# Performance work log

Measured on AMD Instinct MI355X. Metric: run time of the kernel, lower is better.

The kernel has to match this reference:

```python
import jax, jax.numpy as jnp
import numpy as np

B, S, H, T, NF = 64, 512, 1024, 4, 12
P = NF * (NF - 1) // 2  # 66 step pairs


def _head(x, w1, b1, w2, b2):
    # LinearsHead (eval mode: dropout = identity): linear -> relu -> linear
    return jax.nn.relu(x @ w1 + b1) @ w2 + b2


def setup_inputs() -> dict:
    key = jax.random.key(0)
    ks = jax.random.split(key, 12)
    sc = 0.02
    # non-overlapping contiguous spans: targets then facts, each L tokens
    L = S // (T + NF)  # 32
    t_start = jnp.arange(T, dtype=jnp.int32) * L
    f_start = (T + jnp.arange(NF, dtype=jnp.int32)) * L
    target_offsets = jnp.broadcast_to(jnp.stack([t_start, t_start + L], -1), (B, T, 2))
    fact_offsets = jnp.broadcast_to(jnp.stack([f_start, f_start + L], -1), (B, NF, 2))
    return {
        'seq_features': jax.random.normal(ks[0], (B, S, H), jnp.float32),
        'cls_features': jax.random.normal(ks[1], (B, H), jnp.float32),
        'target_offsets': target_offsets,
        'fact_offsets': fact_offsets,
        'fact_score_mask': jnp.ones((B, NF, T), jnp.float32),
        'sentsim_w1': sc * jax.random.normal(ks[2], (2 * H, H), jnp.float32),
        'sentsim_b1': jnp.zeros((H,), jnp.float32),
        'sentsim_w2': sc * jax.random.normal(ks[3], (H, 1), jnp.float32),
        'sentsim_b2': jnp.zeros((1,), jnp.float32),
        'step_w1': sc * jax.random.normal(ks[4], (2 * H, H), jnp.float32),
        'step_b1': jnp.zeros((H,), jnp.float32),
        'step_w2': sc * jax.random.normal(ks[5], (H, 1), jnp.float32),
        'step_b2': jnp.zeros((1,), jnp.float32),
        'state_w1': sc * jax.random.normal(ks[6], (H, H), jnp.float32),
        'state_b1': jnp.zeros((H,), jnp.float32),
        'state_w2': sc * jax.random.normal(ks[7], (H, 1), jnp.float32),
        'state_b2': jnp.zeros((1,), jnp.float32),
        'abd_w1': sc * jax.random.normal(ks[8], (2 * H, H), jnp.float32),
        'abd_b1': jnp.zeros((H,), jnp.float32),
        'abd_w2': sc * jax.random.normal(ks[9], (H, 1), jnp.float32),
        'abd_b2': jnp.zeros((1,), jnp.float32),
        'lambda_weight': jnp.array([0.5, 0.5], jnp.float32),
    }


def reference(seq_features, cls_features, target_offsets, fact_offsets, fact_score_mask,
              sentsim_w1, sentsim_b1, sentsim_w2, sentsim_b2,
              step_w1, step_b1, step_w2, step_b2,
              state_w1, state_b1, state_w2, state_b2,
              abd_w1, abd_b1, abd_w2, abd_b2, lambda_weight):
    b, s, h = seq_features.shape
    t = target_offsets.shape[1]
    nf = fact_offsets.shape[1]
    pos = jnp.arange(s)

    def seg_mean(offs):  # offs [b,k,2] -> mean-pooled [b,k,h]
        m = ((pos >= offs[..., 0:1]) & (pos < offs[..., 1:2])).astype(seq_features.dtype)
        cnt = (offs[..., 1] - offs[..., 0]).astype(seq_features.dtype)[..., None]
        return jnp.einsum('bks,bsh->bkh', m, seq_features) / cnt

    tgt = seg_mean(target_offsets)  # [b,t,h]
    fct = seg_mean(fact_offsets)    # [b,nf,h]

    # fact-cls pairs ordered target-major: features[ti*nf+fi] = cat(fact, target)
    ff = jnp.broadcast_to(fct[:, None], (b, t, nf, h))
    tt = jnp.broadcast_to(tgt[:, :, None], (b, t, nf, h))
    pair = jnp.concatenate([ff, tt], -1).reshape(b, t * nf, 2 * h)
    fact_score = jax.nn.sigmoid(_head(pair, sentsim_w1, sentsim_b1, sentsim_w2, sentsim_b2)[..., 0])  # [b, t*nf]
    # original does .view(len(facts), len(targets)) on the flat t-major scores
    mat = fact_score.reshape(b, nf, t)
    max_per_fact = jnp.max(mat * fact_score_mask, axis=2)  # [b, nf]
    state_fact = jnp.mean(max_per_fact, axis=1)            # [b]
    state_cls = jax.nn.sigmoid(_head(cls_features, state_w1, state_b1, state_w2, state_b2)[..., 0])
    w = jax.nn.softmax(lambda_weight)
    state = w[0] * state_fact + w[1] * state_cls           # [b]

    # step pairs: combinations(range(nf), 2) == row-major triu indices
    i1, i2 = jnp.triu_indices(nf, k=1)
    step_feat = jnp.concatenate([fct[:, i1], fct[:, i2]], -1)  # [b,P,2h]
    step = _head(step_feat, step_w1, step_b1, step_w2, step_b2)[..., 0]  # [b,P]

    tside = jnp.mean(tgt, axis=1)  # sum/len over targets [b,h]
    abd_feat = jnp.concatenate([jnp.broadcast_to(tside[:, None], (b, nf, h)), fct], -1)
    abd = _head(abd_feat, abd_w1, abd_b1, abd_w2, abd_b2)[..., 0]  # [b,nf]

    # step_func == 'softmax_all': joint softmax over step + abd scores
    allsc = jax.nn.softmax(jnp.concatenate([step, abd], axis=1), axis=1)
    np_pairs = i1.shape[0]
    step, abd = allsc[:, :np_pairs], allsc[:, np_pairs:]

    # pack: [state | fact_score | step | step_abd]
    return jnp.concatenate([state[:, None], fact_score, step, abd], axis=1)
```

## Files before the change

kernel.cpp:

```cpp
#include <hip/hip_runtime.h>
#include <hip/hip_bf16.h>

#define B_    64
#define S_    512
#define H_    1024
#define HH_   (H_*H_)
#define T_    4
#define NF_   12
#define TNF_  48
#define NP_   66
#define OUTC_ 127

#define NSENT_ (B_*TNF_)
#define NSTEP_ (B_*NP_)
#define NABD_  (B_*NF_)
#define NCLS_  (B_)
#define NWAVES_ (NSENT_+NSTEP_+NABD_+NCLS_)

#define AROW_FCT   0
#define AROW_TGT   768
#define AROW_TSD   1024
#define AROW_CLS   1088
#define AROWS_     1152

#define GROW_FSENT 0
#define GROW_S1    768
#define GROW_S2    1536
#define GROW_AF    2304
#define GROW_TSENT 3072
#define GROW_AT    3328
#define GROW_CLS   3392
#define GROWS_     3456

typedef __bf16 bf16x8 __attribute__((ext_vector_type(8)));
typedef float  f32x4  __attribute__((ext_vector_type(4)));
typedef __attribute__((address_space(1))) const unsigned int gcu32;
typedef __attribute__((address_space(3))) unsigned int lu32;

__device__ __forceinline__ ushort f2bf(float x) {
    union { float f; unsigned u; } c; c.f = x;
    unsigned r = c.u + 0x7fffu + ((c.u >> 16) & 1u);
    return (ushort)(r >> 16);
}
__device__ __forceinline__ float bflo(unsigned u) {
    union { unsigned u; float f; } c; c.u = u << 16; return c.f;
}
__device__ __forceinline__ float bfhi(unsigned u) {
    union { unsigned u; float f; } c; c.u = u & 0xffff0000u; return c.f;
}

__global__ __launch_bounds__(256) void seg_mean_kernel(
    const float* __restrict__ seq, const int* __restrict__ toffs,
    const int* __restrict__ foffs, float* __restrict__ tgt32,
    ushort* __restrict__ Abf)
{
    int blk = blockIdx.x;
    int b = blk >> 4;
    int k = blk & 15;
    int start, end, arow;
    float* dst32 = nullptr;
    if (k < T_) {
        start = toffs[(b*T_ + k)*2];
        end   = toffs[(b*T_ + k)*2 + 1];
        dst32 = tgt32 + (size_t)(b*T_ + k) * H_;
        arow  = AROW_TGT + b*T_ + k;
    } else {
        int f = k - T_;
        start = foffs[(b*NF_ + f)*2];
        end   = foffs[(b*NF_ + f)*2 + 1];
        arow  = AROW_FCT + b*NF_ + f;
    }
    int h0 = threadIdx.x * 4;
    const float* base = seq + ((size_t)b * S_ + start) * H_ + h0;
    float4 s = make_float4(0.f, 0.f, 0.f, 0.f);
    int n = end - start;
    for (int r = 0; r < n; ++r) {
        float4 v = *(const float4*)(base + (size_t)r * H_);
        s.x += v.x; s.y += v.y; s.z += v.z; s.w += v.w;
    }
    float inv = 1.f / (float)n;
    s.x *= inv; s.y *= inv; s.z *= inv; s.w *= inv;
    if (dst32) *(float4*)(dst32 + h0) = s;
    ushort4 q; q.x = f2bf(s.x); q.y = f2bf(s.y); q.z = f2bf(s.z); q.w = f2bf(s.w);
    *(ushort4*)(Abf + (size_t)arow * H_ + h0) = q;
}

__global__ __launch_bounds__(256) void tside_cls_kernel(
    const float* __restrict__ tgt32, const float* __restrict__ cls,
    ushort* __restrict__ Abf)
{
    int b = blockIdx.x;
    int h0 = threadIdx.x * 4;
    float4 s = make_float4(0.f, 0.f, 0.f, 0.f);
    for (int t = 0; t < T_; ++t) {
        float4 v = *(const float4*)(tgt32 + (size_t)(b*T_ + t)*H_ + h0);
        s.x += v.x; s.y += v.y; s.z += v.z; s.w += v.w;
    }
    ushort4 q;
    q.x = f2bf(s.x*0.25f); q.y = f2bf(s.y*0.25f);
    q.z = f2bf(s.z*0.25f); q.w = f2bf(s.w*0.25f);
    *(ushort4*)(Abf + (size_t)(AROW_TSD + b) * H_ + h0) = q;
    float4 c = *(const float4*)(cls + (size_t)b * H_ + h0);
    ushort4 qc; qc.x = f2bf(c.x); qc.y = f2bf(c.y); qc.z = f2bf(c.z); qc.w = f2bf(c.w);
    *(ushort4*)(Abf + (size_t)(AROW_CLS + b) * H_ + h0) = qc;
}

__global__ __launch_bounds__(256) void transpose_cast_kernel(
    const float* __restrict__ sw1, const float* __restrict__ pw1,
    const float* __restrict__ aw1, const float* __restrict__ cw1,
    ushort* __restrict__ Wt)
{
    __shared__ float Tt[32][33];
    int z = blockIdx.z;
    const float* src;
    switch (z) {
        case 0: src = sw1; break;
        case 1: src = pw1; break;
        case 2: src = pw1 + HH_; break;
        case 3: src = aw1 + HH_; break;
        case 4: src = sw1 + HH_; break;
        case 5: src = aw1; break;
        default: src = cw1; break;
    }
    int k0 = blockIdx.x * 32;
    int n0 = blockIdx.y * 32;
    int tid = threadIdx.x;
    int ty = tid >> 3, tx = tid & 7;
    float4 v = *(const float4*)(src + (size_t)(k0 + ty) * H_ + n0 + tx*4);
    Tt[ty][tx*4 + 0] = v.x; Tt[ty][tx*4 + 1] = v.y;
    Tt[ty][tx*4 + 2] = v.z; Tt[ty][tx*4 + 3] = v.w;
    __syncthreads();
    int nx = ty, kx = tx;
    ushort4 q;
    q.x = f2bf(Tt[kx*4 + 0][nx]); q.y = f2bf(Tt[kx*4 + 1][nx]);
    q.z = f2bf(Tt[kx*4 + 2][nx]); q.w = f2bf(Tt[kx*4 + 3][nx]);
    *(ushort4*)(Wt + (size_t)z * HH_ + (size_t)(n0 + nx) * H_ + k0 + kx*4) = q;
}

__global__ __launch_bounds__(256) void gemm_bf16_kernel(
    const ushort* __restrict__ Abf, const ushort* __restrict__ Wt,
    ushort* __restrict__ G)
{
    __shared__ __align__(16) ushort As[64*32];
    __shared__ __align__(16) ushort Bs[64*32];

    int bx = blockIdx.x;
    int arow_base, wsel, grow_base, mt;
    if (bx < 48)      { int j = bx / 12; mt = bx % 12; arow_base = AROW_FCT; wsel = j; grow_base = j * 768; }
    else if (bx < 52) { mt = bx - 48; arow_base = AROW_TGT; wsel = 4; grow_base = GROW_TSENT; }
    else if (bx == 52){ mt = 0; arow_base = AROW_TSD; wsel = 5; grow_base = GROW_AT; }
    else              { mt = 0; arow_base = AROW_CLS; wsel = 6; grow_base = GROW_CLS; }

    const int tid  = threadIdx.x;
    const int lane = tid & 63;
    const int w    = tid >> 6;
    const int wr   = w >> 1, wc = w & 1;
    const int m0   = mt * 64;
    const int n0   = blockIdx.y * 64;

    const int srow   = lane >> 2;
    const int scol8  = (lane & 3) * 8;
    const ushort* gA = Abf + (size_t)(arow_base + m0 + w*16 + srow) * H_ + scol8;
    const ushort* gB = Wt + (size_t)wsel * HH_ + (size_t)(n0 + w*16 + srow) * H_ + scol8;
    ushort* ldsA = As + w * 512;
    ushort* ldsB = Bs + w * 512;

    f32x4 acc00 = {0.f,0.f,0.f,0.f}, acc01 = {0.f,0.f,0.f,0.f};
    f32x4 acc10 = {0.f,0.f,0.f,0.f}, acc11 = {0.f,0.f,0.f,0.f};

    const int frow = lane & 15;
    const int fk   = (lane >> 4) * 8;
    const ushort* pa = As + (wr*32 + frow) * 32 + fk;
    const ushort* pb = Bs + (wc*32 + frow) * 32 + fk;

    for (int k0 = 0; k0 < H_; k0 += 32) {
        __syncthreads();
        __builtin_amdgcn_global_load_lds((gcu32*)(gA + k0), (lu32*)ldsA, 16, 0, 0);
        __builtin_amdgcn_global_load_lds((gcu32*)(gB + k0), (lu32*)ldsB, 16, 0, 0);
        __syncthreads();

        bf16x8 a0 = *(const bf16x8*)pa;
        bf16x8 a1 = *(const bf16x8*)(pa + 16*32);
        bf16x8 b0 = *(const bf16x8*)pb;
        bf16x8 b1 = *(const bf16x8*)(pb + 16*32);

        acc00 = __builtin_amdgcn_mfma_f32_16x16x32_bf16(a0, b0, acc00, 0, 0, 0);
        acc01 = __builtin_amdgcn_mfma_f32_16x16x32_bf16(a0, b1, acc01, 0, 0, 0);
        acc10 = __builtin_amdgcn_mfma_f32_16x16x32_bf16(a1, b0, acc10, 0, 0, 0);
        acc11 = __builtin_amdgcn_mfma_f32_16x16x32_bf16(a1, b1, acc11, 0, 0, 0);
    }

    const int r0 = (lane >> 4) * 4;
    const int c  = lane & 15;
    const size_t rowb = (size_t)(grow_base + m0 + wr*32);
    #pragma unroll
    for (int r = 0; r < 4; ++r) {
        G[(rowb + 0  + r0 + r) * H_ + n0 + wc*32 + 0  + c] = f2bf(acc00[r]);
        G[(rowb + 0  + r0 + r) * H_ + n0 + wc*32 + 16 + c] = f2bf(acc01[r]);
        G[(rowb + 16 + r0 + r) * H_ + n0 + wc*32 + 0  + c] = f2bf(acc10[r]);
        G[(rowb + 16 + r0 + r) * H_ + n0 + wc*32 + 16 + c] = f2bf(acc11[r]);
    }
}

__global__ __launch_bounds__(256) void combine_kernel(
    const ushort* __restrict__ G,
    const float* __restrict__ sb1, const float* __restrict__ sw2,
    const float* __restrict__ pb1, const float* __restrict__ pw2,
    const float* __restrict__ ab1, const float* __restrict__ aw2,
    const float* __restrict__ cb1, const float* __restrict__ cw2,
    float* __restrict__ ssent, float* __restrict__ sstep,
    float* __restrict__ sabd, float* __restrict__ scls)
{
    int wv = blockIdx.x * 4 + (threadIdx.x >> 6);
    int lane = threadIdx.x & 63;
    if (wv >= NWAVES_) return;

    const ushort *U, *V;
    const float *b1, *w2;
    float* outp;
    if (wv < NSENT_) {
        int b = wv / TNF_, q = wv % TNF_;
        int t = q / NF_, f = q % NF_;
        U = G + (size_t)(GROW_FSENT + b*NF_ + f) * H_;
        V = G + (size_t)(GROW_TSENT + b*T_ + t) * H_;
        b1 = sb1; w2 = sw2; outp = ssent + wv;
    } else if (wv < NSENT_ + NSTEP_) {
        int s = wv - NSENT_;
        int b = s / NP_, p = s % NP_;
        int i = 0, rem = p, cnt = NF_ - 1;
        while (rem >= cnt) { rem -= cnt; --cnt; ++i; }
        int j = i + 1 + rem;
        U = G + (size_t)(GROW_S1 + b*NF_ + i) * H_;
        V = G + (size_t)(GROW_S2 + b*NF_ + j) * H_;
        b1 = pb1; w2 = pw2; outp = sstep + s;
    } else if (wv < NSENT_ + NSTEP_ + NABD_) {
        int s = wv - NSENT_ - NSTEP_;
        int b = s / NF_, f = s % NF_;
        U = G + (size_t)(GROW_AT + b) * H_;
        V = G + (size_t)(GROW_AF + b*NF_ + f) * H_;
        b1 = ab1; w2 = aw2; outp = sabd + s;
    } else {
        int b = wv - NSENT_ - NSTEP_ - NABD_;
        U = G + (size_t)(GROW_CLS + b) * H_;
        V = nullptr;
        b1 = cb1; w2 = cw2; outp = scls + b;
    }

    float acc = 0.f;
    #pragma unroll
    for (int h = 0; h < 2; ++h) {
        int nb = h * 512 + lane * 8;
        uint4 uu = *(const uint4*)(U + nb);
        float us[8] = { bflo(uu.x), bfhi(uu.x), bflo(uu.y), bfhi(uu.y),
                        bflo(uu.z), bfhi(uu.z), bflo(uu.w), bfhi(uu.w) };
        if (V) {
            uint4 vv = *(const uint4*)(V + nb);
            us[0] += bflo(vv.x); us[1] += bfhi(vv.x);
            us[2] += bflo(vv.y); us[3] += bfhi(vv.y);
            us[4] += bflo(vv.z); us[5] += bfhi(vv.z);
            us[6] += bflo(vv.w); us[7] += bfhi(vv.w);
        }
        float4 bA = *(const float4*)(b1 + nb);
        float4 bB = *(const float4*)(b1 + nb + 4);
        float4 wA = *(const float4*)(w2 + nb);
        float4 wB = *(const float4*)(w2 + nb + 4);
        acc = fmaf(fmaxf(us[0] + bA.x, 0.f), wA.x, acc);
        acc = fmaf(fmaxf(us[1] + bA.y, 0.f), wA.y, acc);
        acc = fmaf(fmaxf(us[2] + bA.z, 0.f), wA.z, acc);
        acc = fmaf(fmaxf(us[3] + bA.w, 0.f), wA.w, acc);
        acc = fmaf(fmaxf(us[4] + bB.x, 0.f), wB.x, acc);
        acc = fmaf(fmaxf(us[5] + bB.y, 0.f), wB.y, acc);
        acc = fmaf(fmaxf(us[6] + bB.z, 0.f), wB.z, acc);
        acc = fmaf(fmaxf(us[7] + bB.w, 0.f), wB.w, acc);
    }
    #pragma unroll
    for (int msk = 1; msk < 64; msk <<= 1)
        acc += __shfl_xor(acc, msk);
    if (lane == 0) *outp = acc;
}

__global__ __launch_bounds__(128) void finalize_kernel(
    const float* __restrict__ s_sent, const float* __restrict__ s_step,
    const float* __restrict__ s_abd, const float* __restrict__ s_cls,
    const float* __restrict__ mask, const float* __restrict__ lam,
    const float* __restrict__ sent_b2, const float* __restrict__ step_b2,
    const float* __restrict__ state_b2, const float* __restrict__ abd_b2,
    float* __restrict__ out)
{
    int b = blockIdx.x;
    int tid = threadIdx.x;
    __shared__ float fs[TNF_];
    __shared__ float sc[NP_ + NF_];
    __shared__ float mpf[NF_];
    __shared__ float smax, ssum;

    if (tid < TNF_) {
        float v = 1.f / (1.f + expf(-(s_sent[b*TNF_ + tid] + sent_b2[0])));
        fs[tid] = v;
        out[(size_t)b*OUTC_ + 1 + tid] = v;
    }
    if (tid < NP_)
        sc[tid] = s_step[b*NP_ + tid] + step_b2[0];
    else if (tid < NP_ + NF_)
        sc[tid] = s_abd[b*NF_ + (tid - NP_)] + abd_b2[0];
    __syncthreads();

    if (tid < NF_) {
        float m = -1e30f;
        for (int j = 0; j < T_; ++j)
            m = fmaxf(m, fs[tid*T_ + j] * mask[((size_t)b*NF_ + tid)*T_ + j]);
        mpf[tid] = m;
    }
    __syncthreads();

    if (tid == 0) {
        float sf = 0.f;
        for (int i = 0; i < NF_; ++i) sf += mpf[i];
        sf *= (1.f / NF_);
        float scls2 = 1.f / (1.f + expf(-(s_cls[b] + state_b2[0])));
        float l0 = lam[0], l1 = lam[1];
        float mx = fmaxf(l0, l1);
        float e0 = expf(l0 - mx), e1 = expf(l1 - mx);
        float w0 = e0 / (e0 + e1);
        out[(size_t)b*OUTC_] = w0 * sf + (1.f - w0) * scls2;
        float m2 = -1e30f;
        for (int i = 0; i < NP_ + NF_; ++i) m2 = fmaxf(m2, sc[i]);
        smax = m2;
    }
    __syncthreads();
    if (tid < NP_ + NF_) sc[tid] = expf(sc[tid] - smax);
    __syncthreads();
    if (tid == 0) {
        float s2 = 0.f;
        for (int i = 0; i < NP_ + NF_; ++i) s2 += sc[i];
        ssum = s2;
    }
    __syncthreads();
    if (tid < NP_ + NF_)
        out[(size_t)b*OUTC_ + 1 + TNF_ + tid] = sc[tid] / ssum;
}

extern "C" void kernel_launch(void* const* d_in, const int* in_sizes, int n_in,
                              void* d_out, int out_size, void* d_ws, size_t ws_size,
                              hipStream_t stream)
{
    (void)in_sizes; (void)n_in; (void)out_size; (void)ws_size;
    const float* seq  = (const float*)d_in[0];
    const float* cls  = (const float*)d_in[1];
    const int*   toff = (const int*)d_in[2];
    const int*   foff = (const int*)d_in[3];
    const float* mask = (const float*)d_in[4];
    const float* sw1  = (const float*)d_in[5];
    const float* sb1  = (const float*)d_in[6];
    const float* sw2  = (const float*)d_in[7];
    const float* sb2  = (const float*)d_in[8];
    const float* pw1  = (const float*)d_in[9];
    const float* pb1  = (const float*)d_in[10];
    const float* pw2  = (const float*)d_in[11];
    const float* pb2  = (const float*)d_in[12];
    const float* cw1  = (const float*)d_in[13];
    const float* cb1  = (const float*)d_in[14];
    const float* cw2  = (const float*)d_in[15];
    const float* cb2  = (const float*)d_in[16];
    const float* aw1  = (const float*)d_in[17];
    const float* ab1  = (const float*)d_in[18];
    const float* aw2  = (const float*)d_in[19];
    const float* ab2  = (const float*)d_in[20];
    const float* lam  = (const float*)d_in[21];

    char* wsb = (char*)d_ws;
    float*  tgt32 = (float*)wsb;
    float*  ssent = (float*)(wsb + (1u<<20));
    float*  sstep = ssent + NSENT_;
    float*  sabd  = sstep + NSTEP_;
    float*  scls  = sabd + NABD_;
    ushort* Abf   = (ushort*)(wsb + (1u<<20) + 32768);
    ushort* Wt    = Abf + (size_t)AROWS_ * H_;
    ushort* G     = Wt + (size_t)7 * HH_;

    seg_mean_kernel<<<B_*(T_ + NF_), 256, 0, stream>>>(seq, toff, foff, tgt32, Abf);
    tside_cls_kernel<<<B_, 256, 0, stream>>>(tgt32, cls, Abf);
    transpose_cast_kernel<<<dim3(32, 32, 7), 256, 0, stream>>>(sw1, pw1, aw1, cw1, Wt);

    gemm_bf16_kernel<<<dim3(54, 16), 256, 0, stream>>>(Abf, Wt, G);

    combine_kernel<<<(NWAVES_ + 3) / 4, 256, 0, stream>>>(
        G, sb1, sw2, pb1, pw2, ab1, aw2, cb1, cw2,
        ssent, sstep, sabd, scls);

    finalize_kernel<<<B_, 128, 0, stream>>>(
        ssent, sstep, sabd, scls, mask, lam, sb2, pb2, cb2, ab2, (float*)d_out);
}
```

Measured before the change: 65.65 us.

## Fuse prep kernels and double-buffer GEMM with wider 128-column tiles

Merges the segment-mean, cls cast and weight transpose-cast kernels into one launch so these independent memory-bound passes can run concurrently. Tside stays a separate small kernel. The bf16 GEMM now double-buffers its LDS staging, issuing the next k-tile's global-to-LDS loads before running MFMAs on the current one. It also widens the N tile to 128, giving 8 MFMAs per wave per step and halving the grid. The wider tile means fewer blocks (432) on a large-CU GPU, which may reduce occupancy.

```diff
diff --git a/kernel.cpp b/kernel.cpp
--- a/kernel.cpp
+++ b/kernel.cpp
@@ -49,45 +49,85 @@
     union { unsigned u; float f; } c; c.u = u & 0xffff0000u; return c.f;
 }
 
-__global__ __launch_bounds__(256) void seg_mean_kernel(
+__global__ __launch_bounds__(256) void prep_kernel(
     const float* __restrict__ seq, const int* __restrict__ toffs,
-    const int* __restrict__ foffs, float* __restrict__ tgt32,
-    ushort* __restrict__ Abf)
+    const int* __restrict__ foffs, const float* __restrict__ cls,
+    const float* __restrict__ sw1, const float* __restrict__ pw1,
+    const float* __restrict__ aw1, const float* __restrict__ cw1,
+    float* __restrict__ tgt32, ushort* __restrict__ Abf,
+    ushort* __restrict__ Wt)
 {
     int blk = blockIdx.x;
-    int b = blk >> 4;
-    int k = blk & 15;
-    int start, end, arow;
-    float* dst32 = nullptr;
-    if (k < T_) {
-        start = toffs[(b*T_ + k)*2];
-        end   = toffs[(b*T_ + k)*2 + 1];
-        dst32 = tgt32 + (size_t)(b*T_ + k) * H_;
-        arow  = AROW_TGT + b*T_ + k;
+    int tid = threadIdx.x;
+
+    if (blk < 1024) {
+        int b = blk >> 4;
+        int k = blk & 15;
+        int start, end, arow;
+        float* dst32 = nullptr;
+        if (k < T_) {
+            start = toffs[(b*T_ + k)*2];
+            end   = toffs[(b*T_ + k)*2 + 1];
+            dst32 = tgt32 + (size_t)(b*T_ + k) * H_;
+            arow  = AROW_TGT + b*T_ + k;
+        } else {
+            int f = k - T_;
+            start = foffs[(b*NF_ + f)*2];
+            end   = foffs[(b*NF_ + f)*2 + 1];
+            arow  = AROW_FCT + b*NF_ + f;
+        }
+        int h0 = tid * 4;
+        const float* base = seq + ((size_t)b * S_ + start) * H_ + h0;
+        float4 s = make_float4(0.f, 0.f, 0.f, 0.f);
+        int n = end - start;
+        #pragma unroll 4
+        for (int r = 0; r < n; ++r) {
+            float4 v = *(const float4*)(base + (size_t)r * H_);
+            s.x += v.x; s.y += v.y; s.z += v.z; s.w += v.w;
+        }
+        float inv = 1.f / (float)n;
+        s.x *= inv; s.y *= inv; s.z *= inv; s.w *= inv;
+        if (dst32) *(float4*)(dst32 + h0) = s;
+        ushort4 q; q.x = f2bf(s.x); q.y = f2bf(s.y); q.z = f2bf(s.z); q.w = f2bf(s.w);
+        *(ushort4*)(Abf + (size_t)arow * H_ + h0) = q;
+    } else if (blk < 1088) {
+        int b = blk - 1024;
+        int h0 = tid * 4;
+        float4 c = *(const float4*)(cls + (size_t)b * H_ + h0);
+        ushort4 qc; qc.x = f2bf(c.x); qc.y = f2bf(c.y); qc.z = f2bf(c.z); qc.w = f2bf(c.w);
+        *(ushort4*)(Abf + (size_t)(AROW_CLS + b) * H_ + h0) = qc;
     } else {
-        int f = k - T_;
-        start = foffs[(b*NF_ + f)*2];
-        end   = foffs[(b*NF_ + f)*2 + 1];
-        arow  = AROW_FCT + b*NF_ + f;
-    }
-    int h0 = threadIdx.x * 4;
-    const float* base = seq + ((size_t)b * S_ + start) * H_ + h0;
-    float4 s = make_float4(0.f, 0.f, 0.f, 0.f);
-    int n = end - start;
-    for (int r = 0; r < n; ++r) {
-        float4 v = *(const float4*)(base + (size_t)r * H_);
-        s.x += v.x; s.y += v.y; s.z += v.z; s.w += v.w;
-    }
-    float inv = 1.f / (float)n;
-    s.x *= inv; s.y *= inv; s.z *= inv; s.w *= inv;
-    if (dst32) *(float4*)(dst32 + h0) = s;
-    ushort4 q; q.x = f2bf(s.x); q.y = f2bf(s.y); q.z = f2bf(s.z); q.w = f2bf(s.w);
-    *(ushort4*)(Abf + (size_t)arow * H_ + h0) = q;
-}
-
-__global__ __launch_bounds__(256) void tside_cls_kernel(
-    const float* __restrict__ tgt32, const float* __restrict__ cls,
-    ushort* __restrict__ Abf)
+        __shared__ float Tt[32][33];
+        int idx2 = blk - 1088;
+        int z = idx2 >> 10;
+        int rem = idx2 & 1023;
+        int k0 = (rem >> 5) * 32;
+        int n0 = (rem & 31) * 32;
+        const float* src;
+        switch (z) {
+            case 0: src = sw1; break;
+            case 1: src = pw1; break;
+            case 2: src = pw1 + HH_; break;
+            case 3: src = aw1 + HH_; break;
+            case 4: src = sw1 + HH_; break;
+            case 5: src = aw1; break;
+            default: src = cw1; break;
+        }
+        int ty = tid >> 3, tx = tid & 7;
+        float4 v = *(const float4*)(src + (size_t)(k0 + ty) * H_ + n0 + tx*4);
+        Tt[ty][tx*4 + 0] = v.x; Tt[ty][tx*4 + 1] = v.y;
+        Tt[ty][tx*4 + 2] = v.z; Tt[ty][tx*4 + 3] = v.w;
+        __syncthreads();
+        int nx = ty, kx = tx;
+        ushort4 q;
+        q.x = f2bf(Tt[kx*4 + 0][nx]); q.y = f2bf(Tt[kx*4 + 1][nx]);
+        q.z = f2bf(Tt[kx*4 + 2][nx]); q.w = f2bf(Tt[kx*4 + 3][nx]);
+        *(ushort4*)(Wt + (size_t)z * HH_ + (size_t)(n0 + nx) * H_ + k0 + kx*4) = q;
+    }
+}
+
+__global__ __launch_bounds__(256) void tside_kernel(
+    const float* __restrict__ tgt32, ushort* __restrict__ Abf)
 {
     int b = blockIdx.x;
     int h0 = threadIdx.x * 4;
@@ -100,49 +140,14 @@
     q.x = f2bf(s.x*0.25f); q.y = f2bf(s.y*0.25f);
     q.z = f2bf(s.z*0.25f); q.w = f2bf(s.w*0.25f);
     *(ushort4*)(Abf + (size_t)(AROW_TSD + b) * H_ + h0) = q;
-    float4 c = *(const float4*)(cls + (size_t)b * H_ + h0);
-    ushort4 qc; qc.x = f2bf(c.x); qc.y = f2bf(c.y); qc.z = f2bf(c.z); qc.w = f2bf(c.w);
-    *(ushort4*)(Abf + (size_t)(AROW_CLS + b) * H_ + h0) = qc;
-}
-
-__global__ __launch_bounds__(256) void transpose_cast_kernel(
-    const float* __restrict__ sw1, const float* __restrict__ pw1,
-    const float* __restrict__ aw1, const float* __restrict__ cw1,
-    ushort* __restrict__ Wt)
-{
-    __shared__ float Tt[32][33];
-    int z = blockIdx.z;
-    const float* src;
-    switch (z) {
-        case 0: src = sw1; break;
-        case 1: src = pw1; break;
-        case 2: src = pw1 + HH_; break;
-        case 3: src = aw1 + HH_; break;
-        case 4: src = sw1 + HH_; break;
-        case 5: src = aw1; break;
-        default: src = cw1; break;
-    }
-    int k0 = blockIdx.x * 32;
-    int n0 = blockIdx.y * 32;
-    int tid = threadIdx.x;
-    int ty = tid >> 3, tx = tid & 7;
-    float4 v = *(const float4*)(src + (size_t)(k0 + ty) * H_ + n0 + tx*4);
-    Tt[ty][tx*4 + 0] = v.x; Tt[ty][tx*4 + 1] = v.y;
-    Tt[ty][tx*4 + 2] = v.z; Tt[ty][tx*4 + 3] = v.w;
-    __syncthreads();
-    int nx = ty, kx = tx;
-    ushort4 q;
-    q.x = f2bf(Tt[kx*4 + 0][nx]); q.y = f2bf(Tt[kx*4 + 1][nx]);
-    q.z = f2bf(Tt[kx*4 + 2][nx]); q.w = f2bf(Tt[kx*4 + 3][nx]);
-    *(ushort4*)(Wt + (size_t)z * HH_ + (size_t)(n0 + nx) * H_ + k0 + kx*4) = q;
 }
 
 __global__ __launch_bounds__(256) void gemm_bf16_kernel(
     const ushort* __restrict__ Abf, const ushort* __restrict__ Wt,
     ushort* __restrict__ G)
 {
-    __shared__ __align__(16) ushort As[64*32];
-    __shared__ __align__(16) ushort Bs[64*32];
+    __shared__ __align__(16) ushort As[2][64*32];
+    __shared__ __align__(16) ushort Bs[2][128*32];
 
     int bx = blockIdx.x;
     int arow_base, wsel, grow_base, mt;
@@ -156,49 +161,72 @@
     const int w    = tid >> 6;
     const int wr   = w >> 1, wc = w & 1;
     const int m0   = mt * 64;
-    const int n0   = blockIdx.y * 64;
-
-    const int srow   = lane >> 2;
-    const int scol8  = (lane & 3) * 8;
-    const ushort* gA = Abf + (size_t)(arow_base + m0 + w*16 + srow) * H_ + scol8;
-    const ushort* gB = Wt + (size_t)wsel * HH_ + (size_t)(n0 + w*16 + srow) * H_ + scol8;
-    ushort* ldsA = As + w * 512;
-    ushort* ldsB = Bs + w * 512;
-
-    f32x4 acc00 = {0.f,0.f,0.f,0.f}, acc01 = {0.f,0.f,0.f,0.f};
-    f32x4 acc10 = {0.f,0.f,0.f,0.f}, acc11 = {0.f,0.f,0.f,0.f};
+    const int n0   = blockIdx.y * 128;
+
+    const int srow  = lane >> 2;
+    const int scol8 = (lane & 3) * 8;
+    const ushort* gA  = Abf + (size_t)(arow_base + m0 + w*16 + srow) * H_ + scol8;
+    const ushort* gB0 = Wt + (size_t)wsel * HH_ + (size_t)(n0 + w*32 + srow) * H_ + scol8;
+    const ushort* gB1 = gB0 + (size_t)16 * H_;
+
+    f32x4 acc00 = {0,0,0,0}, acc01 = {0,0,0,0}, acc02 = {0,0,0,0}, acc03 = {0,0,0,0};
+    f32x4 acc10 = {0,0,0,0}, acc11 = {0,0,0,0}, acc12 = {0,0,0,0}, acc13 = {0,0,0,0};
 
     const int frow = lane & 15;
     const int fk   = (lane >> 4) * 8;
-    const ushort* pa = As + (wr*32 + frow) * 32 + fk;
-    const ushort* pb = Bs + (wc*32 + frow) * 32 + fk;
-
-    for (int k0 = 0; k0 < H_; k0 += 32) {
-        __syncthreads();
-        __builtin_amdgcn_global_load_lds((gcu32*)(gA + k0), (lu32*)ldsA, 16, 0, 0);
-        __builtin_amdgcn_global_load_lds((gcu32*)(gB + k0), (lu32*)ldsB, 16, 0, 0);
-        __syncthreads();
-
+
+    #define STAGE(buf, kk) do {                                                   \
+        __builtin_amdgcn_global_load_lds((gcu32*)(gA  + (kk)), (lu32*)(As[buf] + w*512), 16, 0, 0);          \
+        __builtin_amdgcn_global_load_lds((gcu32*)(gB0 + (kk)), (lu32*)(Bs[buf] + w*1024), 16, 0, 0);         \
+        __builtin_amdgcn_global_load_lds((gcu32*)(gB1 + (kk)), (lu32*)(Bs[buf] + w*1024 + 512), 16, 0, 0);   \
+    } while (0)
+
+    STAGE(0, 0);
+    __syncthreads();
+
+    #pragma unroll 1
+    for (int t = 0; t < 32; ++t) {
+        const int cur = t & 1;
+        if (t < 31) STAGE(cur ^ 1, (t + 1) * 32);
+
+        const ushort* pa = As[cur] + (wr*32 + frow) * 32 + fk;
+        const ushort* pb = Bs[cur] + (wc*64 + frow) * 32 + fk;
         bf16x8 a0 = *(const bf16x8*)pa;
-        bf16x8 a1 = *(const bf16x8*)(pa + 16*32);
+        bf16x8 a1 = *(const bf16x8*)(pa + 512);
         bf16x8 b0 = *(const bf16x8*)pb;
-        bf16x8 b1 = *(const bf16x8*)(pb + 16*32);
+        bf16x8 b1 = *(const bf16x8*)(pb + 512);
+        bf16x8 b2 = *(const bf16x8*)(pb + 1024);
+        bf16x8 b3 = *(const bf16x8*)(pb + 1536);
 
         acc00 = __builtin_amdgcn_mfma_f32_16x16x32_bf16(a0, b0, acc00, 0, 0, 0);
         acc01 = __builtin_amdgcn_mfma_f32_16x16x32_bf16(a0, b1, acc01, 0, 0, 0);
+        acc02 = __builtin_amdgcn_mfma_f32_16x16x32_bf16(a0, b2, acc02, 0, 0, 0);
+        acc03 = __builtin_amdgcn_mfma_f32_16x16x32_bf16(a0, b3, acc03, 0, 0, 0);
         acc10 = __builtin_amdgcn_mfma_f32_16x16x32_bf16(a1, b0, acc10, 0, 0, 0);
         acc11 = __builtin_amdgcn_mfma_f32_16x16x32_bf16(a1, b1, acc11, 0, 0, 0);
-    }
+        acc12 = __builtin_amdgcn_mfma_f32_16x16x32_bf16(a1, b2, acc12, 0, 0, 0);
+        acc13 = __builtin_amdgcn_mfma_f32_16x16x32_bf16(a1, b3, acc13, 0, 0, 0);
+
+        if (t < 31) __syncthreads();
+    }
+    #undef STAGE
 
     const int r0 = (lane >> 4) * 4;
     const int c  = lane & 15;
     const size_t rowb = (size_t)(grow_base + m0 + wr*32);
+    const size_t colb = (size_t)(n0 + wc*64);
     #pragma unroll
     for (int r = 0; r < 4; ++r) {
-        G[(rowb + 0  + r0 + r) * H_ + n0 + wc*32 + 0  + c] = f2bf(acc00[r]);
-        G[(rowb + 0  + r0 + r) * H_ + n0 + wc*32 + 16 + c] = f2bf(acc01[r]);
-        G[(rowb + 16 + r0 + r) * H_ + n0 + wc*32 + 0  + c] = f2bf(acc10[r]);
-        G[(rowb + 16 + r0 + r) * H_ + n0 + wc*32 + 16 + c] = f2bf(acc11[r]);
+        size_t ra = (rowb + r0 + r) * H_ + colb;
+        size_t rb = (rowb + 16 + r0 + r) * H_ + colb;
+        G[ra + 0  + c] = f2bf(acc00[r]);
+        G[ra + 16 + c] = f2bf(acc01[r]);
+        G[ra + 32 + c] = f2bf(acc02[r]);
+        G[ra + 48 + c] = f2bf(acc03[r]);
+        G[rb + 0  + c] = f2bf(acc10[r]);
+        G[rb + 16 + c] = f2bf(acc11[r]);
+        G[rb + 32 + c] = f2bf(acc12[r]);
+        G[rb + 48 + c] = f2bf(acc13[r]);
     }
 }
 
@@ -378,11 +406,12 @@
     ushort* Wt    = Abf + (size_t)AROWS_ * H_;
     ushort* G     = Wt + (size_t)7 * HH_;
 
-    seg_mean_kernel<<<B_*(T_ + NF_), 256, 0, stream>>>(seq, toff, foff, tgt32, Abf);
-    tside_cls_kernel<<<B_, 256, 0, stream>>>(tgt32, cls, Abf);
-    transpose_cast_kernel<<<dim3(32, 32, 7), 256, 0, stream>>>(sw1, pw1, aw1, cw1, Wt);
-
-    gemm_bf16_kernel<<<dim3(54, 16), 256, 0, stream>>>(Abf, Wt, G);
+    prep_kernel<<<1088 + 7*1024, 256, 0, stream>>>(
+        seq, toff, foff, cls, sw1, pw1, aw1, cw1, tgt32, Abf, Wt);
+
+    tside_kernel<<<B_, 256, 0, stream>>>(tgt32, Abf);
+
+    gemm_bf16_kernel<<<dim3(54, 8), 256, 0, stream>>>(Abf, Wt, G);
 
     combine_kernel<<<(NWAVES_ + 3) / 4, 256, 0, stream>>>(
         G, sb1, sw2, pb1, pw2, ab1, aw2, cb1, cw2,
```

Result: no change. 65.25 us (-0.6%).
